# Kernel optimization log

Measured on AMD Instinct MI355X. Metric: run time of the kernel, lower is better.

The kernel has to match this reference:

```python
import jax, jax.numpy as jnp
import numpy as np
from jax import lax

D_MODEL = 1024
D_STATE = 128
HEADDIM = 64
EXPAND = 2
NGROUPS = 1
CHUNK = 256
D_INNER = EXPAND * D_MODEL          # 2048
D_SSM = D_INNER                      # d_ssm defaults to d_inner
NHEADS = D_SSM // HEADDIM            # 32
CONV_DIM = D_SSM + 2 * NGROUPS * D_STATE   # 2304
D_IN_PROJ = 2 * D_INNER + 2 * NGROUPS * D_STATE + NHEADS  # 4384 -> d_mlp = 0
BATCH = 2
SEQLEN = 2048
EPS = 1e-5


def setup_inputs() -> dict:
    key = jax.random.key(0)
    ks = jax.random.split(key, 9)
    u = jax.random.normal(ks[0], (BATCH, SEQLEN, D_MODEL), jnp.float32)
    # indices into left-padded (len = SEQLEN+1) sequence; 0 selects the zero pad
    conv_indices = jax.random.randint(ks[1], (BATCH, 4 * SEQLEN), 0, SEQLEN + 1)
    W_in = jax.random.normal(ks[2], (D_IN_PROJ, D_MODEL), jnp.float32) / np.sqrt(D_MODEL).astype(np.float32)
    conv_w = jax.random.normal(ks[3], (CONV_DIM, 4), jnp.float32) * 0.2
    conv_b = jax.random.normal(ks[4], (CONV_DIM,), jnp.float32) * 0.02
    # dt_bias init exactly as the module: inverse-softplus of dt in [dt_min, dt_max]
    dt = jnp.exp(jax.random.uniform(ks[5], (NHEADS,), jnp.float32) * (np.log(0.1) - np.log(0.001)) + np.log(0.001))
    dt = jnp.clip(dt, 1e-4)
    dt_bias = dt + jnp.log(-jnp.expm1(-dt))
    A_log = jnp.log(jax.random.uniform(ks[6], (NHEADS,), jnp.float32, minval=1.0, maxval=16.0))
    D = jnp.ones((NHEADS,), jnp.float32)
    norm_w = jnp.ones((D_SSM,), jnp.float32)
    W_out = jax.random.normal(ks[7], (D_MODEL, D_INNER), jnp.float32) / np.sqrt(D_INNER).astype(np.float32)
    return dict(u=u, conv_indices=conv_indices, W_in=W_in, conv_w=conv_w, conv_b=conv_b,
                dt_bias=dt_bias, A_log=A_log, D=D, norm_w=norm_w, W_out=W_out)


def _segsum(x):
    # x: (b, c, h, cs) -> (b, c, h, cs, cs); out[..., t, s] = sum_{k=s+1..t} x[..., k]
    cs = x.shape[-1]
    cx = jnp.cumsum(x, axis=-1)
    diff = cx[..., :, None] - cx[..., None, :]
    mask = jnp.tril(jnp.ones((cs, cs), dtype=bool))
    return jnp.where(mask, diff, -jnp.inf)


def _ssd(x, dt, A, Bh, Ch, D):
    # Mamba2 SSD chunked scan. x:(b,l,h,p), dt:(b,l,h), A:(h,), Bh/Ch:(b,l,h,n), D:(h,)
    b, l, h, p = x.shape
    n = Bh.shape[-1]
    c = l // CHUNK
    xr = x.reshape(b, c, CHUNK, h, p)
    dtr = dt.reshape(b, c, CHUNK, h)
    Br = Bh.reshape(b, c, CHUNK, h, n)
    Cr = Ch.reshape(b, c, CHUNK, h, n)
    dA = dtr * A                                 # (b,c,cs,h)
    Acum = jnp.cumsum(dA, axis=2)                # (b,c,cs,h)
    Lm = jnp.exp(_segsum(jnp.transpose(dA, (0, 1, 3, 2))))  # (b,c,h,cs,cs)
    dtx = xr * dtr[..., None]                    # dt-weighted inputs
    # intra-chunk (diagonal blocks)
    Yd = jnp.einsum('bcthn,bcshn,bchts,bcshp->bcthp', Cr, Br, Lm, dtx)
    # per-chunk final states
    decay_states = jnp.exp(Acum[:, :, -1:, :] - Acum)        # (b,c,cs,h)
    states = jnp.einsum('bcshn,bcsh,bcshp->bchpn', Br, decay_states, dtx)
    chunk_decay = jnp.exp(Acum[:, :, -1, :])     # (b,c,h)
    def step(h_prev, inp):
        dec, st = inp
        return h_prev * dec[..., None, None] + st, h_prev
    init = jnp.zeros((b, h, p, n), x.dtype)
    _, prev = lax.scan(step, init, (jnp.moveaxis(chunk_decay, 1, 0), jnp.moveaxis(states, 1, 0)))
    prev = jnp.moveaxis(prev, 0, 1)              # (b,c,h,p,n): state entering each chunk
    # inter-chunk (off-diagonal) contribution
    Yoff = jnp.einsum('bcthn,bchpn,bcth->bcthp', Cr, prev, jnp.exp(Acum))
    Y = Yd + Yoff + D[None, None, None, :, None] * xr
    return Y.reshape(b, l, h, p)


def reference(u, conv_indices, W_in, conv_w, conv_b, dt_bias, A_log, D, norm_w, W_out):
    b, l, _ = u.shape
    zxbcdt = u @ W_in.T                          # (b,l,4384); d_mlp == 0
    z, xBC, dt_raw = jnp.split(zxbcdt, [D_SSM, D_SSM + CONV_DIM], axis=-1)
    # tree conv: left-pad seq by 1, gather 4 tree positions per output step, depthwise conv k=4 stride=4
    xc = jnp.transpose(xBC, (0, 2, 1))           # (b, conv_dim, l)
    xp = jnp.pad(xc, ((0, 0), (0, 0), (1, 0)))
    idx = jnp.broadcast_to(conv_indices[:, None, :], (b, CONV_DIM, 4 * l))
    g = jnp.take_along_axis(xp, idx, axis=2).reshape(b, CONV_DIM, l, 4)
    conv = jnp.einsum('bclk,ck->bcl', g, conv_w) + conv_b[None, :, None]
    xBC = jax.nn.silu(jnp.transpose(conv, (0, 2, 1)))  # (b,l,conv_dim)
    x, Bm, Cm = jnp.split(xBC, [D_SSM, D_SSM + NGROUPS * D_STATE], axis=-1)
    x = x.reshape(b, l, NHEADS, HEADDIM)
    hpg = NHEADS // NGROUPS
    Bh = jnp.repeat(Bm.reshape(b, l, NGROUPS, D_STATE), hpg, axis=2)
    Ch = jnp.repeat(Cm.reshape(b, l, NGROUPS, D_STATE), hpg, axis=2)
    dt = jax.nn.softplus(dt_raw + dt_bias)       # dt_softplus=True, default dt_limit
    A = -jnp.exp(A_log.astype(jnp.float32))
    y = _ssd(x, dt, A, Bh, Ch, D).reshape(b, l, D_SSM)
    # RMSNormGated, norm_before_gate=False, group_size = d_ssm (ngroups=1)
    yz = y * jax.nn.silu(z)
    var = jnp.mean(jnp.square(yz), axis=-1, keepdims=True)
    y = yz * lax.rsqrt(var + EPS) * norm_w
    return y @ W_out.T
```

## Files before the change

### kernel.cpp

```cpp
#include <hip/hip_runtime.h>

#define BB 2
#define LL 2048
#define DMODEL 1024
#define DSSM 2048
#define NH 32
#define HD 64
#define DST 128
#define CONVD 2304
#define DPROJ 4384
#define CS 64
#define NC 32
#define BLTOT (BB*LL)

typedef short v8s __attribute__((ext_vector_type(8)));
typedef float v4f __attribute__((ext_vector_type(4)));

__device__ __forceinline__ float b2f(unsigned short h) {
  union { unsigned int u; float f; } v; v.u = ((unsigned int)h) << 16; return v.f;
}
__device__ __forceinline__ unsigned short f2b(float f) {
  union { float f; unsigned int u; } v; v.f = f;
  unsigned int u = v.u;
  return (unsigned short)((u + 0x7fffu + ((u >> 16) & 1u)) >> 16);
}
__device__ __forceinline__ v4f mfma16(v8s a, v8s b, v4f c) {
  return __builtin_amdgcn_mfma_f32_16x16x32_bf16(a, b, c, 0, 0, 0);
}
__device__ __forceinline__ void gl_lds16(const unsigned short* g, unsigned short* l) {
  __builtin_amdgcn_global_load_lds(
      (const __attribute__((address_space(1))) void*)(g),
      (__attribute__((address_space(3))) void*)(l), 16, 0, 0);
}

__global__ __launch_bounds__(256) void cvt_kernel(const float* __restrict__ in,
                                                  unsigned short* __restrict__ out, int n4) {
  int i = blockIdx.x * 256 + threadIdx.x;
  if (i < n4) {
    float4 v = ((const float4*)in)[i];
    ushort4 o;
    o.x = f2b(v.x); o.y = f2b(v.y); o.z = f2b(v.z); o.w = f2b(v.w);
    ((ushort4*)out)[i] = o;
  }
}

template<int OUT_BF16>
__global__ __launch_bounds__(256) void gemm_bt(
    const unsigned short* __restrict__ A, const unsigned short* __restrict__ Bt,
    void* __restrict__ Cout, int M, int N, int K, int ldc)
{
  const int bm = blockIdx.x, bn = blockIdx.y;
  const int tid = threadIdx.x;
  const int wave = tid >> 6, lane = tid & 63;
  const int wm = wave & 1, wn = wave >> 1;
  const int q = lane >> 4, lr = lane & 15;

  __shared__ __align__(16) unsigned short As[128 * 64];
  __shared__ __align__(16) unsigned short Bs[128 * 64];

  v4f acc[4][4];
#pragma unroll
  for (int i = 0; i < 4; i++)
#pragma unroll
    for (int j = 0; j < 4; j++) acc[i][j] = v4f{0.f, 0.f, 0.f, 0.f};

  const int lrow = lane >> 3;
  const int gchunk = (lane & 7) ^ lrow;

  for (int k0 = 0; k0 < K; k0 += 64) {
    __syncthreads();
#pragma unroll
    for (int it = 0; it < 4; ++it) {
      int r = wave * 32 + it * 8 + lrow;
      const unsigned short* ga = A + (size_t)(bm * 128 + r) * K + k0 + gchunk * 8;
      gl_lds16(ga, &As[(wave * 32 + it * 8) * 64]);
      int rb = bn * 128 + r; if (rb >= N) rb = N - 1;
      const unsigned short* gb = Bt + (size_t)rb * K + k0 + gchunk * 8;
      gl_lds16(gb, &Bs[(wave * 32 + it * 8) * 64]);
    }
    __syncthreads();
#pragma unroll
    for (int ks = 0; ks < 64; ks += 32) {
      const int c0 = (ks >> 3) + q;
      v8s af[4], bf[4];
#pragma unroll
      for (int mt = 0; mt < 4; ++mt) {
        int r = wm * 64 + mt * 16 + lr;
        af[mt] = *(const v8s*)&As[r * 64 + ((c0 ^ (r & 7)) << 3)];
      }
#pragma unroll
      for (int nt = 0; nt < 4; ++nt) {
        int r = wn * 64 + nt * 16 + lr;
        bf[nt] = *(const v8s*)&Bs[r * 64 + ((c0 ^ (r & 7)) << 3)];
      }
#pragma unroll
      for (int mt = 0; mt < 4; ++mt)
#pragma unroll
        for (int nt = 0; nt < 4; ++nt)
          acc[mt][nt] = mfma16(af[mt], bf[nt], acc[mt][nt]);
    }
  }
#pragma unroll
  for (int mt = 0; mt < 4; ++mt) {
#pragma unroll
    for (int nt = 0; nt < 4; ++nt) {
      int row = bm * 128 + wm * 64 + mt * 16 + q * 4;
      int col = bn * 128 + wn * 64 + nt * 16 + lr;
      if (col < N) {
#pragma unroll
        for (int r = 0; r < 4; ++r) {
          float v = acc[mt][nt][r];
          if (OUT_BF16) ((unsigned short*)Cout)[(size_t)(row + r) * ldc + col] = f2b(v);
          else          ((float*)Cout)[(size_t)(row + r) * ldc + col] = v;
        }
      }
    }
  }
}

__global__ __launch_bounds__(256) void conv_kernel(
    const unsigned short* __restrict__ C1, const int* __restrict__ cidx,
    const float* __restrict__ convw, const float* __restrict__ convb,
    const float* __restrict__ dtbias,
    unsigned short* __restrict__ x16, unsigned short* __restrict__ Bg16,
    unsigned short* __restrict__ Cg16, float* __restrict__ dtb)
{
  int bl = blockIdx.x;
  int b = bl >> 11;
  int tid = threadIdx.x;
  __shared__ int idxs[4];
  if (tid < 4) idxs[tid] = cidx[b * (4 * LL) + ((bl & 2047) * 4) + tid];
  __syncthreads();
  const unsigned short* rows[4];
#pragma unroll
  for (int k = 0; k < 4; k++) {
    int iv = idxs[k];
    rows[k] = (iv > 0) ? (C1 + (size_t)(b * LL + iv - 1) * DPROJ + DSSM) : (const unsigned short*)0;
  }
  const float4* cw4 = (const float4*)convw;
  for (int it = 0; it < 9; ++it) {
    int c = tid + it * 256;
    float4 w = cw4[c];
    float acc = convb[c];
    if (rows[0]) acc += b2f(rows[0][c]) * w.x;
    if (rows[1]) acc += b2f(rows[1][c]) * w.y;
    if (rows[2]) acc += b2f(rows[2][c]) * w.z;
    if (rows[3]) acc += b2f(rows[3][c]) * w.w;
    float s = acc / (1.f + __expf(-acc));
    unsigned short sv = f2b(s);
    if (c < DSSM)            x16[(size_t)bl * DSSM + c] = sv;
    else if (c < DSSM + DST) Bg16[(size_t)bl * DST + (c - DSSM)] = sv;
    else                     Cg16[(size_t)bl * DST + (c - DSSM - DST)] = sv;
  }
  if (tid < NH) {
    float raw = b2f(C1[(size_t)bl * DPROJ + DSSM + CONVD + tid]) + dtbias[tid];
    float dtv = (raw > 20.f) ? raw : log1pf(__expf(raw));
    dtb[(size_t)bl * NH + tid] = dtv;
  }
}

__global__ __launch_bounds__(256) void d1_intra(
    const unsigned short* __restrict__ x16, const unsigned short* __restrict__ Bg16,
    const unsigned short* __restrict__ Cg16, const float* __restrict__ dtb,
    const float* __restrict__ A_log,
    unsigned short* __restrict__ y16, unsigned short* __restrict__ statesb,
    float* __restrict__ cdb, float* __restrict__ acumb)
{
  int gid = blockIdx.x;
  int h = gid & 31, ci = (gid >> 5) & 31, b = gid >> 10;
  int tid = threadIdx.x, wave = tid >> 6, lane = tid & 63, q = lane >> 4, lr = lane & 15;

  __shared__ __align__(16) unsigned short Cn[CS * 136];
  __shared__ __align__(16) unsigned short BnG[CS * 136];
  __shared__ __align__(16) unsigned short BTw[DST * 72];
  __shared__ __align__(16) unsigned short xdtT[HD * 72];
  __shared__ float dt_s[CS], ac_s[CS], dec_s[CS];

  const size_t blbase = (size_t)b * LL + ci * CS;
  float Ah = -__expf(A_log[h]);

  if (tid < CS) {
    float d = dtb[(blbase + tid) * NH + h];
    dt_s[tid] = d;
    ac_s[tid] = d * Ah;
  }
  __syncthreads();

#pragma unroll
  for (int g = 0; g < 8; ++g) {
    int f = g * 256 + tid;
    int s = f >> 5, c4 = (f & 31) * 4;
    *(ushort4*)&BnG[s * 136 + c4] = *(const ushort4*)(Bg16 + (blbase + s) * DST + c4);
    *(ushort4*)&Cn[s * 136 + c4]  = *(const ushort4*)(Cg16 + (blbase + s) * DST + c4);
  }
#pragma unroll
  for (int g = 0; g < 4; ++g) {
    int f = g * 256 + tid;
    int s = f >> 4, p4 = (f & 15) * 4;
    ushort4 xv = *(const ushort4*)(x16 + (blbase + s) * DSSM + h * HD + p4);
    float d = dt_s[s];
    xdtT[(p4 + 0) * 72 + s] = f2b(b2f(xv.x) * d);
    xdtT[(p4 + 1) * 72 + s] = f2b(b2f(xv.y) * d);
    xdtT[(p4 + 2) * 72 + s] = f2b(b2f(xv.z) * d);
    xdtT[(p4 + 3) * 72 + s] = f2b(b2f(xv.w) * d);
  }
  for (int off = 1; off < CS; off <<= 1) {
    float v = 0.f;
    if (tid < CS && tid >= off) v = ac_s[tid - off];
    __syncthreads();
    if (tid < CS && tid >= off) ac_s[tid] += v;
    __syncthreads();
  }
  if (tid < CS) dec_s[tid] = __expf(ac_s[CS - 1] - ac_s[tid]);
  __syncthreads();

#pragma unroll
  for (int g = 0; g < 4; ++g) {
    int f = g * 256 + tid;
    int n = f >> 3, sg = f & 7;
    ushort4 lo, hi;
    {
      int s0 = sg * 8;
      lo.x = f2b(b2f(BnG[(s0 + 0) * 136 + n]) * dec_s[s0 + 0]);
      lo.y = f2b(b2f(BnG[(s0 + 1) * 136 + n]) * dec_s[s0 + 1]);
      lo.z = f2b(b2f(BnG[(s0 + 2) * 136 + n]) * dec_s[s0 + 2]);
      lo.w = f2b(b2f(BnG[(s0 + 3) * 136 + n]) * dec_s[s0 + 3]);
      hi.x = f2b(b2f(BnG[(s0 + 4) * 136 + n]) * dec_s[s0 + 4]);
      hi.y = f2b(b2f(BnG[(s0 + 5) * 136 + n]) * dec_s[s0 + 5]);
      hi.z = f2b(b2f(BnG[(s0 + 6) * 136 + n]) * dec_s[s0 + 6]);
      hi.w = f2b(b2f(BnG[(s0 + 7) * 136 + n]) * dec_s[s0 + 7]);
    }
    *(ushort4*)&BTw[n * 72 + sg * 8] = lo;
    *(ushort4*)&BTw[n * 72 + sg * 8 + 4] = hi;
  }

  v4f accS[4];
#pragma unroll
  for (int i = 0; i < 4; i++) accS[i] = v4f{0.f, 0.f, 0.f, 0.f};
#pragma unroll
  for (int ks = 0; ks < 128; ks += 32) {
    v8s a = *(const v8s*)&Cn[(wave * 16 + lr) * 136 + ks + q * 8];
#pragma unroll
    for (int si = 0; si < 4; ++si) {
      v8s bb = *(const v8s*)&BnG[(si * 16 + lr) * 136 + ks + q * 8];
      accS[si] = mfma16(a, bb, accS[si]);
    }
  }
  __syncthreads();

  {
    int tbase = wave * 16 + q * 4;
#pragma unroll
    for (int si = 0; si < 4; ++si) {
      int s = si * 16 + lr;
#pragma unroll
      for (int r = 0; r < 4; ++r) {
        int tt = tbase + r;
        float g = 0.f;
        if (s <= tt) g = accS[si][r] * __expf(ac_s[tt] - ac_s[s]);
        BnG[tt * 72 + s] = f2b(g);
      }
    }
  }
  __syncthreads();

  v4f accY[4], accP0[4], accP1[4];
#pragma unroll
  for (int i = 0; i < 4; i++) { accY[i] = v4f{0.f,0.f,0.f,0.f}; accP0[i] = v4f{0.f,0.f,0.f,0.f}; accP1[i] = v4f{0.f,0.f,0.f,0.f}; }
  int n0 = wave * 32, n1 = wave * 32 + 16;
#pragma unroll
  for (int ks = 0; ks < 64; ks += 32) {
    v8s aG  = *(const v8s*)&BnG[(wave * 16 + lr) * 72 + ks + q * 8];
    v8s aB0 = *(const v8s*)&BTw[(n0 + lr) * 72 + ks + q * 8];
    v8s aB1 = *(const v8s*)&BTw[(n1 + lr) * 72 + ks + q * 8];
#pragma unroll
    for (int nt = 0; nt < 4; ++nt) {
      v8s bb = *(const v8s*)&xdtT[(nt * 16 + lr) * 72 + ks + q * 8];
      accY[nt]  = mfma16(aG,  bb, accY[nt]);
      accP0[nt] = mfma16(aB0, bb, accP0[nt]);
      accP1[nt] = mfma16(aB1, bb, accP1[nt]);
    }
  }

#pragma unroll
  for (int nt = 0; nt < 4; ++nt) {
    int p = nt * 16 + lr;
#pragma unroll
    for (int r = 0; r < 4; ++r) {
      int t = wave * 16 + q * 4 + r;
      y16[(blbase + t) * DSSM + h * HD + p] = f2b(accY[nt][r]);
    }
  }
  size_t sbase = (((size_t)(b * NC + ci) * NH) + h) * (DST * HD);
#pragma unroll
  for (int nt = 0; nt < 4; ++nt) {
    int p = nt * 16 + lr;
#pragma unroll
    for (int r = 0; r < 4; ++r) {
      int na = n0 + q * 4 + r;
      int nb = n1 + q * 4 + r;
      statesb[sbase + (size_t)na * HD + p] = f2b(accP0[nt][r]);
      statesb[sbase + (size_t)nb * HD + p] = f2b(accP1[nt][r]);
    }
  }
  if (tid == 0) cdb[(b * NC + ci) * NH + h] = __expf(ac_s[CS - 1]);
  if (tid < CS) acumb[((size_t)((b * NC + ci) * NH + h)) * CS + tid] = ac_s[tid];
}

__global__ __launch_bounds__(256) void d2_scan(
    unsigned short* __restrict__ statesb, const float* __restrict__ cdb)
{
  int g = blockIdx.x;
  int part = g & 7, bh = g >> 3;
  int b = bh >> 5, h = bh & 31;
  int tid = threadIdx.x;
  float run[4] = {0.f, 0.f, 0.f, 0.f};
  for (int ci = 0; ci < NC; ++ci) {
    float cd = cdb[(b * NC + ci) * NH + h];
    size_t base = (((size_t)(b * NC + ci) * NH) + h) * (DST * HD) + part * 1024;
#pragma unroll
    for (int i = 0; i < 4; i++) {
      size_t off = base + tid + i * 256;
      float st = b2f(statesb[off]);
      statesb[off] = f2b(run[i]);
      run[i] = run[i] * cd + st;
    }
  }
}

__global__ __launch_bounds__(256) void d3_inter(
    const unsigned short* __restrict__ x16, const unsigned short* __restrict__ Cg16,
    const unsigned short* __restrict__ statesb, const float* __restrict__ acumb,
    const float* __restrict__ Dp, unsigned short* __restrict__ y16)
{
  int gid = blockIdx.x;
  int h = gid & 31, ci = (gid >> 5) & 31, b = gid >> 10;
  int tid = threadIdx.x, wave = tid >> 6, lane = tid & 63, q = lane >> 4, lr = lane & 15;
  __shared__ __align__(16) unsigned short Cn[CS * 136];
  __shared__ __align__(16) unsigned short pT[HD * 136];
  __shared__ float ea[CS];
  const size_t blbase = (size_t)b * LL + ci * CS;
  size_t abase = ((size_t)((b * NC + ci) * NH + h)) * CS;
  if (tid < CS) ea[tid] = __expf(acumb[abase + tid]);
#pragma unroll
  for (int g = 0; g < 8; ++g) {
    int f = g * 256 + tid;
    int s = f >> 5, c4 = (f & 31) * 4;
    *(ushort4*)&Cn[s * 136 + c4] = *(const ushort4*)(Cg16 + (blbase + s) * DST + c4);
  }
  size_t sbase = (((size_t)(b * NC + ci) * NH) + h) * (DST * HD);
#pragma unroll
  for (int g = 0; g < 8; ++g) {
    int f = g * 256 + tid;
    int n = f >> 4, p4 = (f & 15) * 4;
    ushort4 v = *(const ushort4*)(statesb + sbase + (size_t)n * HD + p4);
    pT[(p4 + 0) * 136 + n] = v.x;
    pT[(p4 + 1) * 136 + n] = v.y;
    pT[(p4 + 2) * 136 + n] = v.z;
    pT[(p4 + 3) * 136 + n] = v.w;
  }
  __syncthreads();
  v4f acc[4];
#pragma unroll
  for (int i = 0; i < 4; i++) acc[i] = v4f{0.f, 0.f, 0.f, 0.f};
#pragma unroll
  for (int ks = 0; ks < 128; ks += 32) {
    v8s a = *(const v8s*)&Cn[(wave * 16 + lr) * 136 + ks + q * 8];
#pragma unroll
    for (int nt = 0; nt < 4; ++nt) {
      v8s bb = *(const v8s*)&pT[(nt * 16 + lr) * 136 + ks + q * 8];
      acc[nt] = mfma16(a, bb, acc[nt]);
    }
  }
  float Dh = Dp[h];
#pragma unroll
  for (int nt = 0; nt < 4; ++nt) {
    int p = nt * 16 + lr;
#pragma unroll
    for (int r = 0; r < 4; ++r) {
      int t = wave * 16 + q * 4 + r;
      size_t off = (blbase + t) * DSSM + h * HD + p;
      float yv = b2f(y16[off]) + ea[t] * acc[nt][r] + Dh * b2f(x16[off]);
      y16[off] = f2b(yv);
    }
  }
}

__global__ __launch_bounds__(256) void norm_kernel(
    const unsigned short* __restrict__ y16, const unsigned short* __restrict__ C1,
    const float* __restrict__ normw, unsigned short* __restrict__ yzn)
{
  int bl = blockIdx.x;
  int tid = threadIdx.x;
  int wave = tid >> 6, lane = tid & 63;
  float vals[8];
  float ss = 0.f;
#pragma unroll
  for (int i = 0; i < 8; ++i) {
    int d = tid + i * 256;
    float yv = b2f(y16[(size_t)bl * DSSM + d]);
    float zv = b2f(C1[(size_t)bl * DPROJ + d]);
    float g = zv / (1.f + __expf(-zv));
    float v = yv * g;
    vals[i] = v;
    ss += v * v;
  }
#pragma unroll
  for (int off = 32; off > 0; off >>= 1) ss += __shfl_down(ss, off);
  __shared__ float red[4];
  if (lane == 0) red[wave] = ss;
  __syncthreads();
  float tot = red[0] + red[1] + red[2] + red[3];
  float scale = rsqrtf(tot * (1.f / 2048.f) + 1e-5f);
#pragma unroll
  for (int i = 0; i < 8; ++i) {
    int d = tid + i * 256;
    yzn[(size_t)bl * DSSM + d] = f2b(vals[i] * scale * normw[d]);
  }
}

extern "C" void kernel_launch(void* const* d_in, const int* in_sizes, int n_in,
                              void* d_out, int out_size, void* d_ws, size_t ws_size,
                              hipStream_t stream) {
  const float* u      = (const float*)d_in[0];
  const int*   cidx   = (const int*)d_in[1];
  const float* W_in   = (const float*)d_in[2];
  const float* convw  = (const float*)d_in[3];
  const float* convb  = (const float*)d_in[4];
  const float* dtbias = (const float*)d_in[5];
  const float* A_log  = (const float*)d_in[6];
  const float* Dp     = (const float*)d_in[7];
  const float* normw  = (const float*)d_in[8];
  const float* W_out  = (const float*)d_in[9];

  char* w = (char*)d_ws;
  size_t off = 0;
  auto alloc = [&](size_t bytes) { char* p = w + off; off += (bytes + 255) & ~(size_t)255; return p; };
  unsigned short* u16     = (unsigned short*)alloc((size_t)BLTOT * DMODEL * 2);
  unsigned short* Win16   = (unsigned short*)alloc((size_t)DPROJ * DMODEL * 2);
  unsigned short* Wout16  = (unsigned short*)alloc((size_t)DMODEL * DSSM * 2);
  unsigned short* C1      = (unsigned short*)alloc((size_t)BLTOT * DPROJ * 2);
  unsigned short* x16     = (unsigned short*)alloc((size_t)BLTOT * DSSM * 2);
  unsigned short* Bg16    = (unsigned short*)alloc((size_t)BLTOT * DST * 2);
  unsigned short* Cg16    = (unsigned short*)alloc((size_t)BLTOT * DST * 2);
  float*          dtb     = (float*)alloc((size_t)BLTOT * NH * 4);
  float*          acumb   = (float*)alloc((size_t)BB * NC * NH * CS * 4);
  unsigned short* y16     = (unsigned short*)alloc((size_t)BLTOT * DSSM * 2);
  unsigned short* statesb = (unsigned short*)alloc((size_t)BB * NC * NH * DST * HD * 2);
  float*          cdb     = (float*)alloc((size_t)BB * NC * NH * 4);
  unsigned short* yzn     = (unsigned short*)alloc((size_t)BLTOT * DSSM * 2);

  cvt_kernel<<<(BLTOT * DMODEL / 4 + 255) / 256, 256, 0, stream>>>(u, u16, BLTOT * DMODEL / 4);
  cvt_kernel<<<(DPROJ * DMODEL / 4 + 255) / 256, 256, 0, stream>>>(W_in, Win16, DPROJ * DMODEL / 4);
  cvt_kernel<<<(DMODEL * DSSM / 4 + 255) / 256, 256, 0, stream>>>(W_out, Wout16, DMODEL * DSSM / 4);

  gemm_bt<1><<<dim3(BLTOT / 128, (DPROJ + 127) / 128), 256, 0, stream>>>(
      u16, Win16, C1, BLTOT, DPROJ, DMODEL, DPROJ);
  conv_kernel<<<BLTOT, 256, 0, stream>>>(C1, cidx, convw, convb, dtbias, x16, Bg16, Cg16, dtb);
  d1_intra<<<BB * NC * NH, 256, 0, stream>>>(x16, Bg16, Cg16, dtb, A_log, y16, statesb, cdb, acumb);
  d2_scan<<<BB * NH * 8, 256, 0, stream>>>(statesb, cdb);
  d3_inter<<<BB * NC * NH, 256, 0, stream>>>(x16, Cg16, statesb, acumb, Dp, y16);
  norm_kernel<<<BLTOT, 256, 0, stream>>>(y16, C1, normw, yzn);
  gemm_bt<0><<<dim3(BLTOT / 128, DMODEL / 128), 256, 0, stream>>>(
      yzn, Wout16, (float*)d_out, BLTOT, DMODEL, DSSM, DMODEL);
}
```

Before: 295.8 us.

## Merge conversions, vectorize conv/norm/inter epilogues, and streamline intra-chunk scan

Merges the three fp32-to-bf16 conversion launches into a single kernel. Vectorizes the conv kernel to four channels per thread and the norm kernel to eight, and rewrites the d3_inter epilogue to stage results through LDS so it can do 16-byte loads and stores. In d1_intra, the cumulative-sum scan becomes a single-wave shuffle scan instead of a barrier-heavy LDS scan. The dt scaling moves from x onto the B-side and G matrices, and the C tile is read straight from global memory instead of being staged in LDS. Together these aim to cut launch overhead, barrier count and narrow memory accesses, at the cost of extra LDS in d3 and uncoalesced global fragment reads for C.

```diff
diff --git a/kernel.cpp b/kernel.cpp
--- a/kernel.cpp
+++ b/kernel.cpp
@@ -33,15 +33,21 @@
       (__attribute__((address_space(3))) void*)(l), 16, 0, 0);
 }
 
-__global__ __launch_bounds__(256) void cvt_kernel(const float* __restrict__ in,
-                                                  unsigned short* __restrict__ out, int n4) {
+__global__ __launch_bounds__(256) void cvt3_kernel(
+    const float* __restrict__ a, unsigned short* __restrict__ oa, int na4,
+    const float* __restrict__ b, unsigned short* __restrict__ ob, int nb4,
+    const float* __restrict__ c, unsigned short* __restrict__ oc, int nc4)
+{
   int i = blockIdx.x * 256 + threadIdx.x;
-  if (i < n4) {
-    float4 v = ((const float4*)in)[i];
-    ushort4 o;
-    o.x = f2b(v.x); o.y = f2b(v.y); o.z = f2b(v.z); o.w = f2b(v.w);
-    ((ushort4*)out)[i] = o;
-  }
+  const float* src; unsigned short* dst; int j;
+  if (i < na4) { src = a; dst = oa; j = i; }
+  else if (i < na4 + nb4) { src = b; dst = ob; j = i - na4; }
+  else if (i < na4 + nb4 + nc4) { src = c; dst = oc; j = i - na4 - nb4; }
+  else return;
+  float4 v = ((const float4*)src)[j];
+  ushort4 o;
+  o.x = f2b(v.x); o.y = f2b(v.y); o.z = f2b(v.z); o.w = f2b(v.w);
+  ((ushort4*)dst)[j] = o;
 }
 
 template<int OUT_BF16>
@@ -138,19 +144,29 @@
     rows[k] = (iv > 0) ? (C1 + (size_t)(b * LL + iv - 1) * DPROJ + DSSM) : (const unsigned short*)0;
   }
   const float4* cw4 = (const float4*)convw;
-  for (int it = 0; it < 9; ++it) {
-    int c = tid + it * 256;
-    float4 w = cw4[c];
-    float acc = convb[c];
-    if (rows[0]) acc += b2f(rows[0][c]) * w.x;
-    if (rows[1]) acc += b2f(rows[1][c]) * w.y;
-    if (rows[2]) acc += b2f(rows[2][c]) * w.z;
-    if (rows[3]) acc += b2f(rows[3][c]) * w.w;
-    float s = acc / (1.f + __expf(-acc));
-    unsigned short sv = f2b(s);
-    if (c < DSSM)            x16[(size_t)bl * DSSM + c] = sv;
-    else if (c < DSSM + DST) Bg16[(size_t)bl * DST + (c - DSSM)] = sv;
-    else                     Cg16[(size_t)bl * DST + (c - DSSM - DST)] = sv;
+#pragma unroll
+  for (int it = 0; it < 3; ++it) {
+    int unit = tid + it * 256;
+    if (unit >= CONVD / 4) break;
+    int c4 = unit * 4;
+    ushort4 rv[4];
+#pragma unroll
+    for (int k = 0; k < 4; ++k)
+      rv[k] = rows[k] ? *(const ushort4*)(rows[k] + c4) : make_ushort4(0, 0, 0, 0);
+    float4 w0 = cw4[c4], w1 = cw4[c4 + 1], w2 = cw4[c4 + 2], w3 = cw4[c4 + 3];
+    float4 cb = *(const float4*)(convb + c4);
+    float a0 = cb.x + b2f(rv[0].x) * w0.x + b2f(rv[1].x) * w0.y + b2f(rv[2].x) * w0.z + b2f(rv[3].x) * w0.w;
+    float a1 = cb.y + b2f(rv[0].y) * w1.x + b2f(rv[1].y) * w1.y + b2f(rv[2].y) * w1.z + b2f(rv[3].y) * w1.w;
+    float a2 = cb.z + b2f(rv[0].z) * w2.x + b2f(rv[1].z) * w2.y + b2f(rv[2].z) * w2.z + b2f(rv[3].z) * w2.w;
+    float a3 = cb.w + b2f(rv[0].w) * w3.x + b2f(rv[1].w) * w3.y + b2f(rv[2].w) * w3.z + b2f(rv[3].w) * w3.w;
+    ushort4 o;
+    o.x = f2b(a0 / (1.f + __expf(-a0)));
+    o.y = f2b(a1 / (1.f + __expf(-a1)));
+    o.z = f2b(a2 / (1.f + __expf(-a2)));
+    o.w = f2b(a3 / (1.f + __expf(-a3)));
+    if (c4 < DSSM)            *(ushort4*)(x16 + (size_t)bl * DSSM + c4) = o;
+    else if (c4 < DSSM + DST) *(ushort4*)(Bg16 + (size_t)bl * DST + (c4 - DSSM)) = o;
+    else                      *(ushort4*)(Cg16 + (size_t)bl * DST + (c4 - DSSM - DST)) = o;
   }
   if (tid < NH) {
     float raw = b2f(C1[(size_t)bl * DPROJ + DSSM + CONVD + tid]) + dtbias[tid];
@@ -170,68 +186,65 @@
   int h = gid & 31, ci = (gid >> 5) & 31, b = gid >> 10;
   int tid = threadIdx.x, wave = tid >> 6, lane = tid & 63, q = lane >> 4, lr = lane & 15;
 
-  __shared__ __align__(16) unsigned short Cn[CS * 136];
   __shared__ __align__(16) unsigned short BnG[CS * 136];
   __shared__ __align__(16) unsigned short BTw[DST * 72];
-  __shared__ __align__(16) unsigned short xdtT[HD * 72];
+  __shared__ __align__(16) unsigned short xT[HD * 72];
   __shared__ float dt_s[CS], ac_s[CS], dec_s[CS];
 
   const size_t blbase = (size_t)b * LL + ci * CS;
+  const size_t chbase = (size_t)(b * NC + ci) * NH + h;
   float Ah = -__expf(A_log[h]);
 
-  if (tid < CS) {
-    float d = dtb[(blbase + tid) * NH + h];
-    dt_s[tid] = d;
-    ac_s[tid] = d * Ah;
-  }
-  __syncthreads();
+  if (wave == 0) {
+    float d = dtb[(blbase + lane) * NH + h];
+    float a = d * Ah;
+#pragma unroll
+    for (int off = 1; off < 64; off <<= 1) {
+      float u = __shfl_up(a, off, 64);
+      if (lane >= off) a += u;
+    }
+    float tot = __shfl(a, 63, 64);
+    dt_s[lane] = d;
+    ac_s[lane] = a;
+    dec_s[lane] = __expf(tot - a);
+    acumb[chbase * CS + lane] = a;
+    if (lane == 0) cdb[chbase] = __expf(tot);
+  }
 
 #pragma unroll
   for (int g = 0; g < 8; ++g) {
     int f = g * 256 + tid;
     int s = f >> 5, c4 = (f & 31) * 4;
     *(ushort4*)&BnG[s * 136 + c4] = *(const ushort4*)(Bg16 + (blbase + s) * DST + c4);
-    *(ushort4*)&Cn[s * 136 + c4]  = *(const ushort4*)(Cg16 + (blbase + s) * DST + c4);
   }
 #pragma unroll
   for (int g = 0; g < 4; ++g) {
     int f = g * 256 + tid;
     int s = f >> 4, p4 = (f & 15) * 4;
     ushort4 xv = *(const ushort4*)(x16 + (blbase + s) * DSSM + h * HD + p4);
-    float d = dt_s[s];
-    xdtT[(p4 + 0) * 72 + s] = f2b(b2f(xv.x) * d);
-    xdtT[(p4 + 1) * 72 + s] = f2b(b2f(xv.y) * d);
-    xdtT[(p4 + 2) * 72 + s] = f2b(b2f(xv.z) * d);
-    xdtT[(p4 + 3) * 72 + s] = f2b(b2f(xv.w) * d);
-  }
-  for (int off = 1; off < CS; off <<= 1) {
-    float v = 0.f;
-    if (tid < CS && tid >= off) v = ac_s[tid - off];
-    __syncthreads();
-    if (tid < CS && tid >= off) ac_s[tid] += v;
-    __syncthreads();
-  }
-  if (tid < CS) dec_s[tid] = __expf(ac_s[CS - 1] - ac_s[tid]);
+    xT[(p4 + 0) * 72 + s] = xv.x;
+    xT[(p4 + 1) * 72 + s] = xv.y;
+    xT[(p4 + 2) * 72 + s] = xv.z;
+    xT[(p4 + 3) * 72 + s] = xv.w;
+  }
   __syncthreads();
 
 #pragma unroll
   for (int g = 0; g < 4; ++g) {
     int f = g * 256 + tid;
     int n = f >> 3, sg = f & 7;
+    int s0 = sg * 8;
     ushort4 lo, hi;
-    {
-      int s0 = sg * 8;
-      lo.x = f2b(b2f(BnG[(s0 + 0) * 136 + n]) * dec_s[s0 + 0]);
-      lo.y = f2b(b2f(BnG[(s0 + 1) * 136 + n]) * dec_s[s0 + 1]);
-      lo.z = f2b(b2f(BnG[(s0 + 2) * 136 + n]) * dec_s[s0 + 2]);
-      lo.w = f2b(b2f(BnG[(s0 + 3) * 136 + n]) * dec_s[s0 + 3]);
-      hi.x = f2b(b2f(BnG[(s0 + 4) * 136 + n]) * dec_s[s0 + 4]);
-      hi.y = f2b(b2f(BnG[(s0 + 5) * 136 + n]) * dec_s[s0 + 5]);
-      hi.z = f2b(b2f(BnG[(s0 + 6) * 136 + n]) * dec_s[s0 + 6]);
-      hi.w = f2b(b2f(BnG[(s0 + 7) * 136 + n]) * dec_s[s0 + 7]);
-    }
-    *(ushort4*)&BTw[n * 72 + sg * 8] = lo;
-    *(ushort4*)&BTw[n * 72 + sg * 8 + 4] = hi;
+    lo.x = f2b(b2f(BnG[(s0 + 0) * 136 + n]) * dec_s[s0 + 0] * dt_s[s0 + 0]);
+    lo.y = f2b(b2f(BnG[(s0 + 1) * 136 + n]) * dec_s[s0 + 1] * dt_s[s0 + 1]);
+    lo.z = f2b(b2f(BnG[(s0 + 2) * 136 + n]) * dec_s[s0 + 2] * dt_s[s0 + 2]);
+    lo.w = f2b(b2f(BnG[(s0 + 3) * 136 + n]) * dec_s[s0 + 3] * dt_s[s0 + 3]);
+    hi.x = f2b(b2f(BnG[(s0 + 4) * 136 + n]) * dec_s[s0 + 4] * dt_s[s0 + 4]);
+    hi.y = f2b(b2f(BnG[(s0 + 5) * 136 + n]) * dec_s[s0 + 5] * dt_s[s0 + 5]);
+    hi.z = f2b(b2f(BnG[(s0 + 6) * 136 + n]) * dec_s[s0 + 6] * dt_s[s0 + 6]);
+    hi.w = f2b(b2f(BnG[(s0 + 7) * 136 + n]) * dec_s[s0 + 7] * dt_s[s0 + 7]);
+    *(ushort4*)&BTw[n * 72 + s0] = lo;
+    *(ushort4*)&BTw[n * 72 + s0 + 4] = hi;
   }
 
   v4f accS[4];
@@ -239,7 +252,7 @@
   for (int i = 0; i < 4; i++) accS[i] = v4f{0.f, 0.f, 0.f, 0.f};
 #pragma unroll
   for (int ks = 0; ks < 128; ks += 32) {
-    v8s a = *(const v8s*)&Cn[(wave * 16 + lr) * 136 + ks + q * 8];
+    v8s a = *(const v8s*)(Cg16 + (blbase + wave * 16 + lr) * DST + ks + q * 8);
 #pragma unroll
     for (int si = 0; si < 4; ++si) {
       v8s bb = *(const v8s*)&BnG[(si * 16 + lr) * 136 + ks + q * 8];
@@ -253,11 +266,12 @@
 #pragma unroll
     for (int si = 0; si < 4; ++si) {
       int s = si * 16 + lr;
+      float ds = dt_s[s], as = ac_s[s];
 #pragma unroll
       for (int r = 0; r < 4; ++r) {
         int tt = tbase + r;
         float g = 0.f;
-        if (s <= tt) g = accS[si][r] * __expf(ac_s[tt] - ac_s[s]);
+        if (s <= tt) g = accS[si][r] * __expf(ac_s[tt] - as) * ds;
         BnG[tt * 72 + s] = f2b(g);
       }
     }
@@ -275,7 +289,7 @@
     v8s aB1 = *(const v8s*)&BTw[(n1 + lr) * 72 + ks + q * 8];
 #pragma unroll
     for (int nt = 0; nt < 4; ++nt) {
-      v8s bb = *(const v8s*)&xdtT[(nt * 16 + lr) * 72 + ks + q * 8];
+      v8s bb = *(const v8s*)&xT[(nt * 16 + lr) * 72 + ks + q * 8];
       accY[nt]  = mfma16(aG,  bb, accY[nt]);
       accP0[nt] = mfma16(aB0, bb, accP0[nt]);
       accP1[nt] = mfma16(aB1, bb, accP1[nt]);
@@ -291,7 +305,7 @@
       y16[(blbase + t) * DSSM + h * HD + p] = f2b(accY[nt][r]);
     }
   }
-  size_t sbase = (((size_t)(b * NC + ci) * NH) + h) * (DST * HD);
+  size_t sbase = chbase * (DST * HD);
 #pragma unroll
   for (int nt = 0; nt < 4; ++nt) {
     int p = nt * 16 + lr;
@@ -303,8 +317,6 @@
       statesb[sbase + (size_t)nb * HD + p] = f2b(accP1[nt][r]);
     }
   }
-  if (tid == 0) cdb[(b * NC + ci) * NH + h] = __expf(ac_s[CS - 1]);
-  if (tid < CS) acumb[((size_t)((b * NC + ci) * NH + h)) * CS + tid] = ac_s[tid];
 }
 
 __global__ __launch_bounds__(256) void d2_scan(
@@ -336,19 +348,13 @@
   int gid = blockIdx.x;
   int h = gid & 31, ci = (gid >> 5) & 31, b = gid >> 10;
   int tid = threadIdx.x, wave = tid >> 6, lane = tid & 63, q = lane >> 4, lr = lane & 15;
-  __shared__ __align__(16) unsigned short Cn[CS * 136];
   __shared__ __align__(16) unsigned short pT[HD * 136];
+  __shared__ __align__(16) float ys[CS * 68];
   __shared__ float ea[CS];
   const size_t blbase = (size_t)b * LL + ci * CS;
-  size_t abase = ((size_t)((b * NC + ci) * NH + h)) * CS;
-  if (tid < CS) ea[tid] = __expf(acumb[abase + tid]);
-#pragma unroll
-  for (int g = 0; g < 8; ++g) {
-    int f = g * 256 + tid;
-    int s = f >> 5, c4 = (f & 31) * 4;
-    *(ushort4*)&Cn[s * 136 + c4] = *(const ushort4*)(Cg16 + (blbase + s) * DST + c4);
-  }
-  size_t sbase = (((size_t)(b * NC + ci) * NH) + h) * (DST * HD);
+  const size_t chbase = (size_t)(b * NC + ci) * NH + h;
+  if (tid < CS) ea[tid] = __expf(acumb[chbase * CS + tid]);
+  size_t sbase = chbase * (DST * HD);
 #pragma unroll
   for (int g = 0; g < 8; ++g) {
     int f = g * 256 + tid;
@@ -365,24 +371,46 @@
   for (int i = 0; i < 4; i++) acc[i] = v4f{0.f, 0.f, 0.f, 0.f};
 #pragma unroll
   for (int ks = 0; ks < 128; ks += 32) {
-    v8s a = *(const v8s*)&Cn[(wave * 16 + lr) * 136 + ks + q * 8];
+    v8s a = *(const v8s*)(Cg16 + (blbase + wave * 16 + lr) * DST + ks + q * 8);
 #pragma unroll
     for (int nt = 0; nt < 4; ++nt) {
       v8s bb = *(const v8s*)&pT[(nt * 16 + lr) * 136 + ks + q * 8];
       acc[nt] = mfma16(a, bb, acc[nt]);
     }
   }
+#pragma unroll
+  for (int nt = 0; nt < 4; ++nt) {
+#pragma unroll
+    for (int r = 0; r < 4; ++r)
+      ys[(wave * 16 + q * 4 + r) * 68 + nt * 16 + lr] = acc[nt][r];
+  }
+  __syncthreads();
   float Dh = Dp[h];
 #pragma unroll
-  for (int nt = 0; nt < 4; ++nt) {
-    int p = nt * 16 + lr;
-#pragma unroll
-    for (int r = 0; r < 4; ++r) {
-      int t = wave * 16 + q * 4 + r;
-      size_t off = (blbase + t) * DSSM + h * HD + p;
-      float yv = b2f(y16[off]) + ea[t] * acc[nt][r] + Dh * b2f(x16[off]);
-      y16[off] = f2b(yv);
-    }
+  for (int it = 0; it < 2; ++it) {
+    int unit = it * 256 + tid;
+    int t = unit >> 3, p8 = (unit & 7) * 8;
+    float ea_t = ea[t];
+    size_t off = (blbase + t) * DSSM + h * HD + p8;
+    uint4 yv = *(const uint4*)(y16 + off);
+    uint4 xv = *(const uint4*)(x16 + off);
+    float4 o0 = *(const float4*)&ys[t * 68 + p8];
+    float4 o1 = *(const float4*)&ys[t * 68 + p8 + 4];
+    const unsigned int* yu = (const unsigned int*)&yv;
+    const unsigned int* xu = (const unsigned int*)&xv;
+    const float* ov = (const float*)&o0;
+    float oo[8] = {o0.x, o0.y, o0.z, o0.w, o1.x, o1.y, o1.z, o1.w};
+    (void)ov;
+    unsigned int ro[4];
+#pragma unroll
+    for (int d = 0; d < 4; ++d) {
+      unsigned short y0 = (unsigned short)(yu[d] & 0xffffu), y1 = (unsigned short)(yu[d] >> 16);
+      unsigned short x0 = (unsigned short)(xu[d] & 0xffffu), x1 = (unsigned short)(xu[d] >> 16);
+      float v0 = b2f(y0) + ea_t * oo[d * 2 + 0] + Dh * b2f(x0);
+      float v1 = b2f(y1) + ea_t * oo[d * 2 + 1] + Dh * b2f(x1);
+      ro[d] = (unsigned int)f2b(v0) | ((unsigned int)f2b(v1) << 16);
+    }
+    *(uint4*)(y16 + off) = make_uint4(ro[0], ro[1], ro[2], ro[3]);
   }
 }
 
@@ -393,17 +421,22 @@
   int bl = blockIdx.x;
   int tid = threadIdx.x;
   int wave = tid >> 6, lane = tid & 63;
+  int c8 = tid * 8;
+  uint4 yv = *(const uint4*)(y16 + (size_t)bl * DSSM + c8);
+  uint4 zv = *(const uint4*)(C1 + (size_t)bl * DPROJ + c8);
+  const unsigned int* yu = (const unsigned int*)&yv;
+  const unsigned int* zu = (const unsigned int*)&zv;
   float vals[8];
   float ss = 0.f;
 #pragma unroll
-  for (int i = 0; i < 8; ++i) {
-    int d = tid + i * 256;
-    float yv = b2f(y16[(size_t)bl * DSSM + d]);
-    float zv = b2f(C1[(size_t)bl * DPROJ + d]);
-    float g = zv / (1.f + __expf(-zv));
-    float v = yv * g;
-    vals[i] = v;
-    ss += v * v;
+  for (int d = 0; d < 4; ++d) {
+    unsigned short y0 = (unsigned short)(yu[d] & 0xffffu), y1 = (unsigned short)(yu[d] >> 16);
+    unsigned short z0 = (unsigned short)(zu[d] & 0xffffu), z1 = (unsigned short)(zu[d] >> 16);
+    float zf0 = b2f(z0), zf1 = b2f(z1);
+    float v0 = b2f(y0) * (zf0 / (1.f + __expf(-zf0)));
+    float v1 = b2f(y1) * (zf1 / (1.f + __expf(-zf1)));
+    vals[d * 2] = v0; vals[d * 2 + 1] = v1;
+    ss += v0 * v0 + v1 * v1;
   }
 #pragma unroll
   for (int off = 32; off > 0; off >>= 1) ss += __shfl_down(ss, off);
@@ -412,11 +445,17 @@
   __syncthreads();
   float tot = red[0] + red[1] + red[2] + red[3];
   float scale = rsqrtf(tot * (1.f / 2048.f) + 1e-5f);
-#pragma unroll
-  for (int i = 0; i < 8; ++i) {
-    int d = tid + i * 256;
-    yzn[(size_t)bl * DSSM + d] = f2b(vals[i] * scale * normw[d]);
-  }
+  float4 w0 = *(const float4*)(normw + c8);
+  float4 w1 = *(const float4*)(normw + c8 + 4);
+  float ws[8] = {w0.x, w0.y, w0.z, w0.w, w1.x, w1.y, w1.z, w1.w};
+  unsigned int ro[4];
+#pragma unroll
+  for (int d = 0; d < 4; ++d) {
+    unsigned short r0 = f2b(vals[d * 2] * scale * ws[d * 2]);
+    unsigned short r1 = f2b(vals[d * 2 + 1] * scale * ws[d * 2 + 1]);
+    ro[d] = (unsigned int)r0 | ((unsigned int)r1 << 16);
+  }
+  *(uint4*)(yzn + (size_t)bl * DSSM + c8) = make_uint4(ro[0], ro[1], ro[2], ro[3]);
 }
 
 extern "C" void kernel_launch(void* const* d_in, const int* in_sizes, int n_in,
@@ -450,9 +489,9 @@
   float*          cdb     = (float*)alloc((size_t)BB * NC * NH * 4);
   unsigned short* yzn     = (unsigned short*)alloc((size_t)BLTOT * DSSM * 2);
 
-  cvt_kernel<<<(BLTOT * DMODEL / 4 + 255) / 256, 256, 0, stream>>>(u, u16, BLTOT * DMODEL / 4);
-  cvt_kernel<<<(DPROJ * DMODEL / 4 + 255) / 256, 256, 0, stream>>>(W_in, Win16, DPROJ * DMODEL / 4);
-  cvt_kernel<<<(DMODEL * DSSM / 4 + 255) / 256, 256, 0, stream>>>(W_out, Wout16, DMODEL * DSSM / 4);
+  const int na4 = BLTOT * DMODEL / 4, nb4 = DPROJ * DMODEL / 4, nc4 = DMODEL * DSSM / 4;
+  cvt3_kernel<<<(na4 + nb4 + nc4 + 255) / 256, 256, 0, stream>>>(
+      u, u16, na4, W_in, Win16, nb4, W_out, Wout16, nc4);
 
   gemm_bt<1><<<dim3(BLTOT / 128, (DPROJ + 127) / 128), 256, 0, stream>>>(
       u16, Win16, C1, BLTOT, DPROJ, DMODEL, DPROJ);
```

Measured after the change: 272.8 us. 1.08x faster.
